# Optimization experiments

Measured on AMD Instinct MI355X. Metric: run time of the kernel, lower is better.

## Reference

```python
import jax, jax.numpy as jnp
import numpy as np

B, T, N, D = 4, 16, 1024, 128
LN_EPS = 1e-5


def setup_inputs() -> dict:
    key = jax.random.key(0)
    k1, k2, k3 = jax.random.split(key, 3)
    X = jax.random.normal(k1, (B, T, N, D), dtype=jnp.float32)
    # normalized adjacency (dense, values in [0,1))
    A = jax.random.uniform(k2, (N, N), dtype=jnp.float32)
    # GCN linear weight (torch nn.Linear, bias=False): out = x @ W.T
    W = jax.random.normal(k3, (D, D), dtype=jnp.float32) / np.sqrt(D)
    gamma = jnp.ones((D,), dtype=jnp.float32)
    beta = jnp.zeros((D,), dtype=jnp.float32)
    return {"X": X, "A": A, "W": W, "gamma": gamma, "beta": beta}


def reference(X, A, W, gamma, beta):
    d = X.shape[-1]
    inv_sqrt_d_a = np.float32(1.0 / np.sqrt(d + 1e-8))  # score scale
    inv_sqrt_d_b = np.float32(1.0 / np.sqrt(d + 1e-9))  # output scale
    # dynamic attention-like scores over nodes: (b,T,N,N)
    scores = jnp.einsum('btnd,btmd->btnm', X, X)
    St = jax.nn.softmax(scores, axis=-1) * inv_sqrt_d_a  # dropout p=0 => identity
    Aeff = A * St                                        # adjacency-masked attention
    # GCN: relu((Aeff @ X) @ W.T)
    h = jnp.einsum('btnm,btmd->btnd', Aeff, X)
    h = jax.nn.relu(h @ W.T) * inv_sqrt_d_b
    # LayerNorm over last dim
    mu = jnp.mean(h, axis=-1, keepdims=True)
    var = jnp.mean(jnp.square(h - mu), axis=-1, keepdims=True)
    h = (h - mu) * jax.lax.rsqrt(var + LN_EPS) * gamma + beta
    # residual
    return h + X
```

## Files before the change

### kernel.cpp

```cpp
#include <hip/hip_runtime.h>


#define NNODES 1024
#define DDIM   128
#define BROWS  128
#define WROWS  16
#define MC     64
#define NCHUNK (NNODES / MC)
#define THREADS 512

#define CA 0.08838834764831845f
#define CB 0.08838834764831845f
#define LN_EPS 1e-5f

typedef __attribute__((ext_vector_type(8))) short bf16x8;
typedef __attribute__((ext_vector_type(4))) float f32x4;

#define XBF_S 136
#define XBT_S 72
#define P_S   72
#define H_S   136
#define XBF_OFF 0
#define XBT_OFF 8704
#define P_OFF   17920
#define SM_TOT  27136

__device__ __forceinline__ unsigned short f2bf(float f) {
  unsigned int u = __float_as_uint(f);
  u += 0x7FFFu + ((u >> 16) & 1u);
  return (unsigned short)(u >> 16);
}

__device__ __forceinline__ bf16x8 pack8(float4 a, float4 b) {
  union { bf16x8 v; unsigned short u[8]; } pk;
  pk.u[0] = f2bf(a.x); pk.u[1] = f2bf(a.y); pk.u[2] = f2bf(a.z); pk.u[3] = f2bf(a.w);
  pk.u[4] = f2bf(b.x); pk.u[5] = f2bf(b.y); pk.u[6] = f2bf(b.z); pk.u[7] = f2bf(b.w);
  return pk.v;
}

__global__ __launch_bounds__(THREADS, 4)
void sdgcn_fused(const float* __restrict__ X, const float* __restrict__ A,
                 const float* __restrict__ W, const float* __restrict__ gamma,
                 const float* __restrict__ beta, float* __restrict__ Out) {
  const int bt   = blockIdx.x;
  const int row0 = blockIdx.y * BROWS;
  const int tid  = (int)threadIdx.x;
  const int wid  = tid >> 6;
  const int lane = tid & 63;
  const int c    = lane & 15;
  const int q    = lane >> 4;

  const float* Xbt = X + (size_t)bt * NNODES * DDIM;

  __shared__ __align__(16) unsigned short sm[SM_TOT];
  unsigned short* Pw = sm + P_OFF + wid * (WROWS * P_S);

  const int wswz = 16 * (q >> 1);
  const int rswz = 16 * ((c >> 3) & 1);

  bf16x8 qfrag[4];
  float cn[4];
  {
    const float* qrow = Xbt + (size_t)(row0 + wid * WROWS + c) * DDIM;
    float ss = 0.f;
#pragma unroll
    for (int ds = 0; ds < 4; ++ds) {
      const float* p = qrow + ds * 32 + q * 8;
      float4 a = *(const float4*)p;
      float4 b = *(const float4*)(p + 4);
      ss += a.x*a.x + a.y*a.y + a.z*a.z + a.w*a.w;
      ss += b.x*b.x + b.y*b.y + b.z*b.z + b.w*b.w;
      qfrag[ds] = pack8(a, b);
    }
    ss += __shfl_xor(ss, 16, 64);
    ss += __shfl_xor(ss, 32, 64);
#pragma unroll
    for (int r = 0; r < 4; ++r)
      cn[r] = __shfl(ss, (lane & 48) + ((lane & 48) >> 2) + r, 64);
  }

  float z_st[4] = {0.f, 0.f, 0.f, 0.f};
  f32x4 Ofr[8];
#pragma unroll
  for (int dt = 0; dt < 8; ++dt) Ofr[dt] = (f32x4){0.f, 0.f, 0.f, 0.f};

  const int grow = row0 + wid * WROWS + q * 4;

  const int sm_ = tid >> 5, sd4 = tid & 31;
  float4 stg[4];
#pragma unroll
  for (int k = 0; k < 4; ++k)
    stg[k] = *(const float4*)(Xbt + (size_t)(sm_ + k * 16) * DDIM + sd4 * 4);

  for (int ch = 0; ch < NCHUNK; ++ch) {
    const int m0 = ch * MC;
#pragma unroll
    for (int k = 0; k < 4; ++k) {
      float4 v = stg[k];
      unsigned int lo = (unsigned int)f2bf(v.x) | ((unsigned int)f2bf(v.y) << 16);
      unsigned int hi = (unsigned int)f2bf(v.z) | ((unsigned int)f2bf(v.w) << 16);
      *(uint2*)(sm + XBF_OFF + (sm_ + k * 16) * XBF_S + sd4 * 4) = make_uint2(lo, hi);
    }
    __syncthreads();
    if (ch + 1 < NCHUNK) {
      const float* nx = Xbt + (size_t)(m0 + MC) * DDIM;
#pragma unroll
      for (int k = 0; k < 4; ++k)
        stg[k] = *(const float4*)(nx + (size_t)(sm_ + k * 16) * DDIM + sd4 * 4);
    }
    float av[4][4];
#pragma unroll
    for (int r = 0; r < 4; ++r)
#pragma unroll
      for (int mt = 0; mt < 4; ++mt)
        av[r][mt] = A[(size_t)(grow + r) * NNODES + m0 + mt*16 + c];
#pragma unroll
    for (int k = 0; k < 2; ++k) {
      int task = tid + k * THREADS;
      int d = task & 127, m8 = task >> 7;
      int base = XBF_OFF + d;
      unsigned int w0 = (unsigned int)sm[base + (m8*8+0)*XBF_S] | ((unsigned int)sm[base + (m8*8+1)*XBF_S] << 16);
      unsigned int w1 = (unsigned int)sm[base + (m8*8+2)*XBF_S] | ((unsigned int)sm[base + (m8*8+3)*XBF_S] << 16);
      unsigned int w2 = (unsigned int)sm[base + (m8*8+4)*XBF_S] | ((unsigned int)sm[base + (m8*8+5)*XBF_S] << 16);
      unsigned int w3 = (unsigned int)sm[base + (m8*8+6)*XBF_S] | ((unsigned int)sm[base + (m8*8+7)*XBF_S] << 16);
      *(uint4*)(sm + XBT_OFF + d * XBT_S + m8 * 8) = make_uint4(w0, w1, w2, w3);
    }
    f32x4 S[4];
#pragma unroll
    for (int mt = 0; mt < 4; ++mt) {
      f32x4 acc = (f32x4){0.f, 0.f, 0.f, 0.f};
#pragma unroll
      for (int ds = 0; ds < 4; ++ds) {
        bf16x8 bf = *(const bf16x8*)(sm + XBF_OFF + (mt*16 + c) * XBF_S + ds*32 + q*8);
        acc = __builtin_amdgcn_mfma_f32_16x16x32_bf16(qfrag[ds], bf, acc, 0, 0, 0);
      }
      S[mt] = acc;
    }
    __syncthreads();
#pragma unroll
    for (int r = 0; r < 4; ++r) {
      float zr = 0.f;
#pragma unroll
      for (int mt = 0; mt < 4; ++mt) {
        float p = __expf(S[mt][r] - cn[r]);
        zr += p;
        Pw[(q*4 + r) * P_S + (((mt*16) ^ wswz) + c)] = f2bf(p * av[r][mt]);
      }
      z_st[r] += zr;
    }
#pragma unroll
    for (int ks = 0; ks < 2; ++ks) {
      bf16x8 pf = *(const bf16x8*)(Pw + c * P_S + (((ks*32 + q*8) ^ rswz)));
#pragma unroll
      for (int dt = 0; dt < 8; ++dt) {
        bf16x8 vf = *(const bf16x8*)(sm + XBT_OFF + (dt*16 + c) * XBT_S + ks*32 + q*8);
        Ofr[dt] = __builtin_amdgcn_mfma_f32_16x16x32_bf16(pf, vf, Ofr[dt], 0, 0, 0);
      }
    }
  }

#pragma unroll
  for (int r = 0; r < 4; ++r) {
    float z = z_st[r];
#pragma unroll
    for (int off = 1; off < 16; off <<= 1) z += __shfl_xor(z, off, 64);
    z_st[r] = z;
  }

  __syncthreads();
  unsigned short* Hw = sm + XBT_OFF + wid * (WROWS * H_S);
#pragma unroll
  for (int r = 0; r < 4; ++r) {
    float rinv = CA / z_st[r];
#pragma unroll
    for (int dt = 0; dt < 8; ++dt)
      Hw[(q*4 + r) * H_S + (((dt*16) ^ wswz) + c)] = f2bf(Ofr[dt][r] * rinv);
  }
  f32x4 G[8];
#pragma unroll
  for (int jt = 0; jt < 8; ++jt) G[jt] = (f32x4){0.f, 0.f, 0.f, 0.f};
#pragma unroll
  for (int ks = 0; ks < 4; ++ks) {
    bf16x8 hf = *(const bf16x8*)(Hw + c * H_S + (((ks*32 + q*8) ^ rswz)));
#pragma unroll
    for (int jt = 0; jt < 8; ++jt) {
      const float* wr = W + (size_t)(jt*16 + c) * DDIM + ks*32 + q*8;
      float4 a = *(const float4*)wr;
      float4 b = *(const float4*)(wr + 4);
      bf16x8 wf = pack8(a, b);
      G[jt] = __builtin_amdgcn_mfma_f32_16x16x32_bf16(hf, wf, G[jt], 0, 0, 0);
    }
  }
#pragma unroll
  for (int jt = 0; jt < 8; ++jt) {
#pragma unroll
    for (int r = 0; r < 4; ++r) G[jt][r] = fmaxf(G[jt][r], 0.f) * CB;
  }
  float* Obt = Out + (size_t)bt * NNODES * DDIM;
#pragma unroll
  for (int r = 0; r < 4; ++r) {
    float s1 = 0.f, s2 = 0.f;
#pragma unroll
    for (int jt = 0; jt < 8; ++jt) { float v = G[jt][r]; s1 += v; s2 += v * v; }
#pragma unroll
    for (int off = 1; off < 16; off <<= 1) {
      s1 += __shfl_xor(s1, off, 64);
      s2 += __shfl_xor(s2, off, 64);
    }
    float mu = s1 * (1.f / 128.f);
    float va = s2 * (1.f / 128.f) - mu * mu;
    float rs = rsqrtf(va + LN_EPS);
    const float* xr = Xbt + (size_t)(grow + r) * DDIM;
    float* orow = Obt + (size_t)(grow + r) * DDIM;
#pragma unroll
    for (int jt = 0; jt < 8; ++jt) {
      int col = jt * 16 + c;
      orow[col] = (G[jt][r] - mu) * rs * gamma[col] + beta[col] + xr[col];
    }
  }
}

extern "C" void kernel_launch(void* const* d_in, const int* in_sizes, int n_in,
                              void* d_out, int out_size, void* d_ws, size_t ws_size,
                              hipStream_t stream) {
  const float* X     = (const float*)d_in[0];
  const float* A     = (const float*)d_in[1];
  const float* W     = (const float*)d_in[2];
  const float* gamma = (const float*)d_in[3];
  const float* beta  = (const float*)d_in[4];
  float* Out = (float*)d_out;
  dim3 grid(64, NNODES / BROWS);
  hipLaunchKernelGGL(sdgcn_fused, grid, dim3(THREADS), 0, stream, X, A, W, gamma, beta, Out);
}
```

Baseline: 179.7 us.

## Use transposed LDS reads and double-buffered tiled X layout, dropping explicit transpose

Stores each bf16 X chunk in a tiled LDS layout, double-buffered by chunk parity so the second barrier per chunk can be dropped. The V operand is read with ds_read_b64_tr_b16 instead of building a separate transposed copy of X through scalar LDS gathers. It also swaps the MFMA operand order so each lane holds four consecutive columns of one row, which allows float4 loads of A and packed 64-bit stores of P. The cost is inline asm with a full lgkmcnt wait and a sched_barrier, which may limit how well the compiler can overlap LDS reads with MFMA work.

```diff
diff --git a/kernel.cpp b/kernel.cpp
--- a/kernel.cpp
+++ b/kernel.cpp
@@ -15,15 +15,41 @@
 
 typedef __attribute__((ext_vector_type(8))) short bf16x8;
 typedef __attribute__((ext_vector_type(4))) float f32x4;
-
-#define XBF_S 136
-#define XBT_S 72
-#define P_S   72
-#define H_S   136
-#define XBF_OFF 0
-#define XBT_OFF 8704
-#define P_OFF   17920
-#define SM_TOT  27136
+typedef __attribute__((ext_vector_type(2))) unsigned int u32x2;
+
+#define STILE(s) (64*(s))
+
+#define XB0_OFF 0
+#define XB1_OFF 8192
+#define P_OFF   16384
+#define P_S     72
+#define H_S     136
+#define SM_TOT  25600
+
+#define TRREAD16(T, AP)                                                     \
+  asm volatile(                                                             \
+    "ds_read_b64_tr_b16 %0, %16 offset:0\n\t"                               \
+    "ds_read_b64_tr_b16 %1, %16 offset:128\n\t"                             \
+    "ds_read_b64_tr_b16 %2, %16 offset:2048\n\t"                            \
+    "ds_read_b64_tr_b16 %3, %16 offset:2176\n\t"                            \
+    "ds_read_b64_tr_b16 %4, %16 offset:4096\n\t"                            \
+    "ds_read_b64_tr_b16 %5, %16 offset:4224\n\t"                            \
+    "ds_read_b64_tr_b16 %6, %16 offset:6144\n\t"                            \
+    "ds_read_b64_tr_b16 %7, %16 offset:6272\n\t"                            \
+    "ds_read_b64_tr_b16 %8, %16 offset:8192\n\t"                            \
+    "ds_read_b64_tr_b16 %9, %16 offset:8320\n\t"                            \
+    "ds_read_b64_tr_b16 %10, %16 offset:10240\n\t"                          \
+    "ds_read_b64_tr_b16 %11, %16 offset:10368\n\t"                          \
+    "ds_read_b64_tr_b16 %12, %16 offset:12288\n\t"                          \
+    "ds_read_b64_tr_b16 %13, %16 offset:12416\n\t"                          \
+    "ds_read_b64_tr_b16 %14, %16 offset:14336\n\t"                          \
+    "ds_read_b64_tr_b16 %15, %16 offset:14464\n\t"                          \
+    "s_waitcnt lgkmcnt(0)"                                                  \
+    : "=&v"(T[0]), "=&v"(T[1]), "=&v"(T[2]), "=&v"(T[3]),                   \
+      "=&v"(T[4]), "=&v"(T[5]), "=&v"(T[6]), "=&v"(T[7]),                   \
+      "=&v"(T[8]), "=&v"(T[9]), "=&v"(T[10]), "=&v"(T[11]),                 \
+      "=&v"(T[12]), "=&v"(T[13]), "=&v"(T[14]), "=&v"(T[15])                \
+    : "v"(AP))
 
 __device__ __forceinline__ unsigned short f2bf(float f) {
   unsigned int u = __float_as_uint(f);
@@ -49,20 +75,19 @@
   const int lane = tid & 63;
   const int c    = lane & 15;
   const int q    = lane >> 4;
+  const int c2 = c >> 2, c3 = c & 3, q1 = q & 1, q2 = q >> 1;
 
   const float* Xbt = X + (size_t)bt * NNODES * DDIM;
 
-  __shared__ __align__(16) unsigned short sm[SM_TOT];
+  __shared__ __align__(128) unsigned short sm[SM_TOT];
   unsigned short* Pw = sm + P_OFF + wid * (WROWS * P_S);
 
-  const int wswz = 16 * (q >> 1);
-  const int rswz = 16 * ((c >> 3) & 1);
+  const int pswz = 16 * ((c >> 3) & 1);
 
   bf16x8 qfrag[4];
-  float cn[4];
+  float ss = 0.f;
   {
     const float* qrow = Xbt + (size_t)(row0 + wid * WROWS + c) * DDIM;
-    float ss = 0.f;
 #pragma unroll
     for (int ds = 0; ds < 4; ++ds) {
       const float* p = qrow + ds * 32 + q * 8;
@@ -74,114 +99,111 @@
     }
     ss += __shfl_xor(ss, 16, 64);
     ss += __shfl_xor(ss, 32, 64);
-#pragma unroll
-    for (int r = 0; r < 4; ++r)
-      cn[r] = __shfl(ss, (lane & 48) + ((lane & 48) >> 2) + r, 64);
-  }
-
-  float z_st[4] = {0.f, 0.f, 0.f, 0.f};
+  }
+
+  float z_acc = 0.f;
   f32x4 Ofr[8];
 #pragma unroll
   for (int dt = 0; dt < 8; ++dt) Ofr[dt] = (f32x4){0.f, 0.f, 0.f, 0.f};
 
   const int grow = row0 + wid * WROWS + q * 4;
-
-  const int sm_ = tid >> 5, sd4 = tid & 31;
+  const int arow = row0 + wid * WROWS + c;
+
+  const int h4  = tid & 15;
+  const int mlo = (tid >> 4) & 3;
+  const int sd4 = h4 + 16 * (wid & 1);
+  const int mh0 = wid >> 1;
+
   float4 stg[4];
 #pragma unroll
   for (int k = 0; k < 4; ++k)
-    stg[k] = *(const float4*)(Xbt + (size_t)(sm_ + k * 16) * DDIM + sd4 * 4);
+    stg[k] = *(const float4*)(Xbt + (size_t)(mlo + 4*(mh0 + 4*k)) * DDIM + sd4 * 4);
 
   for (int ch = 0; ch < NCHUNK; ++ch) {
     const int m0 = ch * MC;
+    unsigned short* xb = sm + ((ch & 1) ? XB1_OFF : XB0_OFF);
+    const unsigned trb = (unsigned)(size_t)xb + 256u*q + 8u*c;
 #pragma unroll
     for (int k = 0; k < 4; ++k) {
       float4 v = stg[k];
       unsigned int lo = (unsigned int)f2bf(v.x) | ((unsigned int)f2bf(v.y) << 16);
       unsigned int hi = (unsigned int)f2bf(v.z) | ((unsigned int)f2bf(v.w) << 16);
-      *(uint2*)(sm + XBF_OFF + (sm_ + k * 16) * XBF_S + sd4 * 4) = make_uint2(lo, hi);
+      const int s = (sd4 >> 2) * 16 + (mh0 + 4*k);
+      *(uint2*)(xb + STILE(s) + 16*mlo + 4*(sd4 & 3)) = make_uint2(lo, hi);
     }
     __syncthreads();
     if (ch + 1 < NCHUNK) {
       const float* nx = Xbt + (size_t)(m0 + MC) * DDIM;
 #pragma unroll
       for (int k = 0; k < 4; ++k)
-        stg[k] = *(const float4*)(nx + (size_t)(sm_ + k * 16) * DDIM + sd4 * 4);
-    }
-    float av[4][4];
-#pragma unroll
-    for (int r = 0; r < 4; ++r)
-#pragma unroll
-      for (int mt = 0; mt < 4; ++mt)
-        av[r][mt] = A[(size_t)(grow + r) * NNODES + m0 + mt*16 + c];
-#pragma unroll
-    for (int k = 0; k < 2; ++k) {
-      int task = tid + k * THREADS;
-      int d = task & 127, m8 = task >> 7;
-      int base = XBF_OFF + d;
-      unsigned int w0 = (unsigned int)sm[base + (m8*8+0)*XBF_S] | ((unsigned int)sm[base + (m8*8+1)*XBF_S] << 16);
-      unsigned int w1 = (unsigned int)sm[base + (m8*8+2)*XBF_S] | ((unsigned int)sm[base + (m8*8+3)*XBF_S] << 16);
-      unsigned int w2 = (unsigned int)sm[base + (m8*8+4)*XBF_S] | ((unsigned int)sm[base + (m8*8+5)*XBF_S] << 16);
-      unsigned int w3 = (unsigned int)sm[base + (m8*8+6)*XBF_S] | ((unsigned int)sm[base + (m8*8+7)*XBF_S] << 16);
-      *(uint4*)(sm + XBT_OFF + d * XBT_S + m8 * 8) = make_uint4(w0, w1, w2, w3);
-    }
+        stg[k] = *(const float4*)(nx + (size_t)(mlo + 4*(mh0 + 4*k)) * DDIM + sd4 * 4);
+    }
+    float4 av[4];
+#pragma unroll
+    for (int mt = 0; mt < 4; ++mt)
+      av[mt] = *(const float4*)(A + (size_t)arow * NNODES + m0 + mt*16 + 4*q);
     f32x4 S[4];
 #pragma unroll
     for (int mt = 0; mt < 4; ++mt) {
       f32x4 acc = (f32x4){0.f, 0.f, 0.f, 0.f};
 #pragma unroll
       for (int ds = 0; ds < 4; ++ds) {
-        bf16x8 bf = *(const bf16x8*)(sm + XBF_OFF + (mt*16 + c) * XBF_S + ds*32 + q*8);
-        acc = __builtin_amdgcn_mfma_f32_16x16x32_bf16(qfrag[ds], bf, acc, 0, 0, 0);
+        const bf16x8 bf = *(const bf16x8*)(xb + STILE((ds*2 + q2)*16 + mt*4 + c2)
+                                              + 16*c3 + 8*q1);
+        acc = __builtin_amdgcn_mfma_f32_16x16x32_bf16(bf, qfrag[ds], acc, 0, 0, 0);
       }
       S[mt] = acc;
     }
-    __syncthreads();
-#pragma unroll
-    for (int r = 0; r < 4; ++r) {
-      float zr = 0.f;
-#pragma unroll
-      for (int mt = 0; mt < 4; ++mt) {
-        float p = __expf(S[mt][r] - cn[r]);
-        zr += p;
-        Pw[(q*4 + r) * P_S + (((mt*16) ^ wswz) + c)] = f2bf(p * av[r][mt]);
+    float zr = 0.f;
+#pragma unroll
+    for (int mt = 0; mt < 4; ++mt) {
+      float p0 = __expf(S[mt][0] - ss);
+      float p1 = __expf(S[mt][1] - ss);
+      float p2 = __expf(S[mt][2] - ss);
+      float p3 = __expf(S[mt][3] - ss);
+      zr += (p0 + p1) + (p2 + p3);
+      unsigned int lo = (unsigned int)f2bf(p0 * av[mt].x) | ((unsigned int)f2bf(p1 * av[mt].y) << 16);
+      unsigned int hi = (unsigned int)f2bf(p2 * av[mt].z) | ((unsigned int)f2bf(p3 * av[mt].w) << 16);
+      *(uint2*)(Pw + c * P_S + ((mt*16 + 4*q) ^ pswz)) = make_uint2(lo, hi);
+    }
+    z_acc += zr;
+#pragma unroll
+    for (int ks = 0; ks < 2; ++ks) {
+      const bf16x8 pf = *(const bf16x8*)(Pw + c * P_S + ((ks*32 + q*8) ^ pswz));
+      u32x2 T[16];
+      TRREAD16(T, trb + 1024u*ks);
+      __builtin_amdgcn_sched_barrier(0);
+#pragma unroll
+      for (int dt = 0; dt < 8; ++dt) {
+        union { u32x2 d[2]; bf16x8 v; } u;
+        u.d[0] = T[2*dt]; u.d[1] = T[2*dt + 1];
+        Ofr[dt] = __builtin_amdgcn_mfma_f32_16x16x32_bf16(pf, u.v, Ofr[dt], 0, 0, 0);
       }
-      z_st[r] += zr;
-    }
-#pragma unroll
-    for (int ks = 0; ks < 2; ++ks) {
-      bf16x8 pf = *(const bf16x8*)(Pw + c * P_S + (((ks*32 + q*8) ^ rswz)));
-#pragma unroll
-      for (int dt = 0; dt < 8; ++dt) {
-        bf16x8 vf = *(const bf16x8*)(sm + XBT_OFF + (dt*16 + c) * XBT_S + ks*32 + q*8);
-        Ofr[dt] = __builtin_amdgcn_mfma_f32_16x16x32_bf16(pf, vf, Ofr[dt], 0, 0, 0);
-      }
-    }
-  }
-
+    }
+  }
+
+  z_acc += __shfl_xor(z_acc, 16, 64);
+  z_acc += __shfl_xor(z_acc, 32, 64);
+  float zrow[4];
+#pragma unroll
+  for (int r = 0; r < 4; ++r)
+    zrow[r] = __shfl(z_acc, (lane & 48) + ((lane & 48) >> 2) + r, 64);
+
+  __syncthreads();
+  unsigned short* Hw = sm + wid * (WROWS * H_S);
 #pragma unroll
   for (int r = 0; r < 4; ++r) {
-    float z = z_st[r];
-#pragma unroll
-    for (int off = 1; off < 16; off <<= 1) z += __shfl_xor(z, off, 64);
-    z_st[r] = z;
-  }
-
-  __syncthreads();
-  unsigned short* Hw = sm + XBT_OFF + wid * (WROWS * H_S);
-#pragma unroll
-  for (int r = 0; r < 4; ++r) {
-    float rinv = CA / z_st[r];
+    float rinv = CA / zrow[r];
 #pragma unroll
     for (int dt = 0; dt < 8; ++dt)
-      Hw[(q*4 + r) * H_S + (((dt*16) ^ wswz) + c)] = f2bf(Ofr[dt][r] * rinv);
+      Hw[(q*4 + r) * H_S + (((dt*16) ^ (16*(q>>1))) + c)] = f2bf(Ofr[dt][r] * rinv);
   }
   f32x4 G[8];
 #pragma unroll
   for (int jt = 0; jt < 8; ++jt) G[jt] = (f32x4){0.f, 0.f, 0.f, 0.f};
 #pragma unroll
   for (int ks = 0; ks < 4; ++ks) {
-    bf16x8 hf = *(const bf16x8*)(Hw + c * H_S + (((ks*32 + q*8) ^ rswz)));
+    bf16x8 hf = *(const bf16x8*)(Hw + c * H_S + ((ks*32 + q*8) ^ pswz));
 #pragma unroll
     for (int jt = 0; jt < 8; ++jt) {
       const float* wr = W + (size_t)(jt*16 + c) * DDIM + ks*32 + q*8;
```

Result: slower. 201.0 us (+11.9%).
